# Kernel tuning notes

Measured on AMD Instinct MI355X. Metric: run time of the kernel, lower is better.

The kernel has to match this reference:

```python
import jax, jax.numpy as jnp
import numpy as np
from jax import lax

H = 128

def _lstm_gates(x, h, c, w_ih, w_hh, b_ih, b_hh):
    # PyTorch gate order: i, f, g, o
    g = x @ w_ih.T + h @ w_hh.T + b_ih + b_hh
    i, f, gg, o = jnp.split(g, 4, axis=-1)
    c_new = jax.nn.sigmoid(f) * c + jax.nn.sigmoid(i) * jnp.tanh(gg)
    h_new = jax.nn.sigmoid(o) * jnp.tanh(c_new)
    return h_new, c_new

def _lstm_layer(x_btF, w_ih, w_hh, b_ih, b_hh):
    B = x_btF.shape[0]
    h0 = jnp.zeros((B, H), x_btF.dtype)
    c0 = jnp.zeros((B, H), x_btF.dtype)
    def step(carry, xt):
        h, c = carry
        h, c = _lstm_gates(xt, h, c, w_ih, w_hh, b_ih, b_hh)
        return (h, c), h
    (h_T, c_T), ys = lax.scan(step, (h0, c0), jnp.swapaxes(x_btF, 0, 1))
    return jnp.swapaxes(ys, 0, 1), h_T, c_T

def setup_inputs() -> dict:
    key = jax.random.key(0)
    ks = jax.random.split(key, 20)
    B, T, D, P = 4096, 200, 2, 3
    s = 1.0 / np.sqrt(H)
    u = lambda k, shp: jax.random.uniform(k, shp, jnp.float32, -s, s)
    return {
        'x_hist': jax.random.normal(ks[0], (B, T, D), jnp.float32),
        'params': jax.random.normal(ks[1], (B, P), jnp.float32),
        'pred_len': 200,
        'w_ih0': u(ks[2], (4 * H, D)), 'w_hh0': u(ks[3], (4 * H, H)),
        'b_ih0': u(ks[4], (4 * H,)), 'b_hh0': u(ks[5], (4 * H,)),
        'w_ih1': u(ks[6], (4 * H, H)), 'w_hh1': u(ks[7], (4 * H, H)),
        'b_ih1': u(ks[8], (4 * H,)), 'b_hh1': u(ks[9], (4 * H,)),
        'dec_w_ih': u(ks[10], (4 * H, D + P)), 'dec_w_hh': u(ks[11], (4 * H, H)),
        'dec_b_ih': u(ks[12], (4 * H,)), 'dec_b_hh': u(ks[13], (4 * H,)),
        'proj_w': u(ks[14], (H, P)), 'proj_b': u(ks[15], (H,)),
        'out_w': u(ks[16], (2, H)), 'out_b': u(ks[17], (2,)),
    }

def reference(x_hist, params, pred_len, w_ih0, w_hh0, b_ih0, b_hh0,
              w_ih1, w_hh1, b_ih1, b_hh1, dec_w_ih, dec_w_hh, dec_b_ih,
              dec_b_hh, proj_w, proj_b, out_w, out_b):
    # 2-layer encoder LSTM; only last layer's final (h, c) are used
    y1, _, _ = _lstm_layer(x_hist, w_ih0, w_hh0, b_ih0, b_hh0)
    _, h_n, c_n = _lstm_layer(y1, w_ih1, w_hh1, b_ih1, b_hh1)
    h = h_n + params @ proj_w.T + proj_b
    c = c_n
    cur = x_hist[:, -1, :]
    def step(carry, _):
        h, c, cur = carry
        inp = jnp.concatenate([cur, params], axis=-1)
        h, c = _lstm_gates(inp, h, c, dec_w_ih, dec_w_hh, dec_b_ih, dec_b_hh)
        cur = h @ out_w.T + out_b
        return (h, c, cur), cur
    _, preds = lax.scan(step, (h, c, cur), None, length=pred_len)
    return jnp.swapaxes(preds, 0, 1)  # [B, pred_len, 2]
```

## Files before the change

kernel.cpp:

```cpp
#include <hip/hip_runtime.h>
#include <stdint.h>

typedef __bf16 bf16x8 __attribute__((ext_vector_type(8)));
typedef float  f32x4  __attribute__((ext_vector_type(4)));

#define PRED   200
#define TSTEPS 200
#define NBLK   256

#define ASTR   280
#define ALO    136
#define ABUFE  (16*ASTR*2)
#define W_BYTES 131072
#define A_OFF   W_BYTES
#define LDS_A   (A_OFF + 2*ABUFE)
#define STG_OFF (A_OFF + 2*ABUFE)
#define LDS_C   (STG_OFF + ABUFE)

#define ABUFD  8192
#define LDS_D  (2*ABUFD)

#define STATE_FLOATS ((size_t)NBLK*4*2048)

__device__ __forceinline__ float sigm(float x){ return 1.0f/(1.0f+__expf(-x)); }
__device__ __forceinline__ float tanhx(float x){
  float t=__expf(-2.0f*fabsf(x)); float y=(1.0f-t)/(1.0f+t); return copysignf(y,x);
}
__device__ __forceinline__ bf16x8 hi8(float4 a, float4 b){
  bf16x8 r; r[0]=(__bf16)a.x; r[1]=(__bf16)a.y; r[2]=(__bf16)a.z; r[3]=(__bf16)a.w;
  r[4]=(__bf16)b.x; r[5]=(__bf16)b.y; r[6]=(__bf16)b.z; r[7]=(__bf16)b.w; return r;
}
__device__ __forceinline__ bf16x8 lo8(float4 a, float4 b, bf16x8 h){
  bf16x8 r;
  r[0]=(__bf16)(a.x-(float)h[0]); r[1]=(__bf16)(a.y-(float)h[1]);
  r[2]=(__bf16)(a.z-(float)h[2]); r[3]=(__bf16)(a.w-(float)h[3]);
  r[4]=(__bf16)(b.x-(float)h[4]); r[5]=(__bf16)(b.y-(float)h[5]);
  r[6]=(__bf16)(b.z-(float)h[6]); r[7]=(__bf16)(b.w-(float)h[7]); return r;
}
#define MFMA(A,B,C) __builtin_amdgcn_mfma_f32_16x16x32_bf16((A),(B),(C),0,0,0)

__device__ __forceinline__ int aoff(int row, int col){
  return row*512 + ((((col>>3) ^ (row&7)) << 4) | ((col&7)<<1));
}
__device__ __forceinline__ int frdoff(int c, int qd, int kt, int plane){
  return c*512 + (((((kt<<2)+qd) ^ (c&7)) | (plane<<4)) << 4);
}

__global__ void __launch_bounds__(512,2)
k_l0(const float* __restrict__ xh, const float* __restrict__ wih0,
     const float* __restrict__ whh0, const float* __restrict__ bih0,
     const float* __restrict__ bhh0, float* __restrict__ wsf,
     int chunkStart, int chunkLen, unsigned long long stageFloats)
{
  extern __shared__ char smem[];
  const int tid=threadIdx.x, wv=tid>>6, l=tid&63, c=l&15, qd=l>>4;
  const int hc=wv*16+c, blk=blockIdx.x, r0=blk*16;
  float* stf = wsf + stageFloats;
  #pragma unroll
  for (int i=0;i<16;++i){
    int f=i*8+wv, ntg=f>>2, kt=f&3;
    int g=(ntg&3)*128+(ntg>>2)*16+c, k=kt*32+qd*8;
    const float* s=whh0+g*128+k;
    *(bf16x8*)(smem+f*1024+l*16)=hi8(*(const float4*)s,*(const float4*)(s+4));
  }
  bf16x8 wlo[16];
  #pragma unroll
  for (int tt=0;tt<4;++tt)
    #pragma unroll
    for (int kt=0;kt<4;++kt){
      const float* s=whh0+(size_t)(tt*128+hc)*128+kt*32+qd*8;
      float4 a=*(const float4*)s, b=*(const float4*)(s+4);
      wlo[tt*4+kt]=lo8(a,b,hi8(a,b));
    }
  float b0[4], w0x[4], w0y[4];
  #pragma unroll
  for (int tt=0;tt<4;++tt){
    int g=tt*128+hc;
    b0[tt]=bih0[g]+bhh0[g]; w0x[tt]=wih0[2*g]; w0y[tt]=wih0[2*g+1];
  }
  float c0[4];
  {
    __bf16* B1=(__bf16*)(smem+A_OFF+ABUFE);
    const float* hst=stf+(size_t)(blk*4+0)*2048;
    const float* cst=stf+(size_t)(blk*4+1)*2048;
    #pragma unroll
    for (int i=0;i<4;++i){
      int e=tid*4+i, row=e>>7, col=e&127;
      float v=0.f; if(chunkStart) v=hst[e];
      __bf16 h=(__bf16)v;
      B1[row*ASTR+col]=h; B1[row*ASTR+ALO+col]=(__bf16)(v-(float)h);
    }
    #pragma unroll
    for (int j=0;j<4;++j){ float v=0.f; if(chunkStart) v=cst[(qd*4+j)*128+hc]; c0[j]=v; }
  }
  __syncthreads();
  float hprev[4];
  for (int t=0;t<chunkLen;++t){
    const int p=t&1, tg=chunkStart+t;
    if (t){
      float* h0p=wsf+((size_t)(t-1)*NBLK+blk)*2048;
      #pragma unroll
      for (int j=0;j<4;++j) h0p[(qd*4+j)*128+hc]=hprev[j];
    }
    float2 xv[4];
    #pragma unroll
    for (int j=0;j<4;++j) xv[j]=*(const float2*)(xh+(size_t)(r0+qd*4+j)*400+tg*2);
    f32x4 acc[4];
    #pragma unroll
    for (int tt=0;tt<4;++tt) acc[tt]=(f32x4){b0[tt],b0[tt],b0[tt],b0[tt]};
    const char* Ar=smem+A_OFF+(size_t)(1-p)*ABUFE;
    #pragma unroll
    for (int kt=0;kt<4;++kt){
      bf16x8 ah=*(const bf16x8*)(Ar+(c*ASTR+kt*32+qd*8)*2);
      bf16x8 al=*(const bf16x8*)(Ar+(c*ASTR+ALO+kt*32+qd*8)*2);
      #pragma unroll
      for (int tt=0;tt<4;++tt){
        bf16x8 bh=*(const bf16x8*)(smem+(size_t)((wv*4+tt)*4+kt)*1024+l*16);
        acc[tt]=MFMA(ah,bh,acc[tt]);
        acc[tt]=MFMA(al,bh,acc[tt]);
        acc[tt]=MFMA(ah,wlo[tt*4+kt],acc[tt]);
      }
    }
    __bf16* Aw=(__bf16*)(smem+A_OFF+(size_t)p*ABUFE);
    #pragma unroll
    for (int j=0;j<4;++j){
      float gi=acc[0][j]+xv[j].x*w0x[0]+xv[j].y*w0y[0];
      float gf=acc[1][j]+xv[j].x*w0x[1]+xv[j].y*w0y[1];
      float gg=acc[2][j]+xv[j].x*w0x[2]+xv[j].y*w0y[2];
      float go=acc[3][j]+xv[j].x*w0x[3]+xv[j].y*w0y[3];
      float cn=sigm(gf)*c0[j]+sigm(gi)*tanhx(gg); c0[j]=cn;
      float hn=sigm(go)*tanhx(cn);
      int row=qd*4+j;
      __bf16 hh=(__bf16)hn;
      Aw[row*ASTR+hc]=hh; Aw[row*ASTR+ALO+hc]=(__bf16)(hn-(float)hh);
      hprev[j]=hn;
    }
    __syncthreads();
  }
  {
    float* h0p=wsf+((size_t)(chunkLen-1)*NBLK+blk)*2048;
    #pragma unroll
    for (int j=0;j<4;++j){
      int row=qd*4+j;
      h0p[row*128+hc]=hprev[j];
      stf[(size_t)(blk*4+0)*2048+row*128+hc]=hprev[j];
      stf[(size_t)(blk*4+1)*2048+row*128+hc]=c0[j];
    }
  }
}

__global__ void __launch_bounds__(512,2)
k_l1(const float* __restrict__ wih1, const float* __restrict__ whh1,
     const float* __restrict__ bih1, const float* __restrict__ bhh1,
     float* __restrict__ wsf, int chunkStart, int chunkLen,
     unsigned long long stageFloats)
{
  extern __shared__ char smem[];
  const int tid=threadIdx.x, wv=tid>>6, l=tid&63, c=l&15, qd=l>>4;
  const int hc=wv*16+c, blk=blockIdx.x;
  float* stf = wsf + stageFloats;
  #pragma unroll
  for (int i=0;i<16;++i){
    int f=i*8+wv, ntg=f>>2, kt=f&3;
    int g=(ntg&3)*128+(ntg>>2)*16+c, k=kt*32+qd*8;
    const float* s=wih1+g*128+k;
    *(bf16x8*)(smem+f*1024+l*16)=hi8(*(const float4*)s,*(const float4*)(s+4));
  }
  bf16x8 whh[16], whl[16], wil[16];
  #pragma unroll
  for (int tt=0;tt<4;++tt)
    #pragma unroll
    for (int kt=0;kt<4;++kt){
      const float* s2=whh1+(size_t)(tt*128+hc)*128+kt*32+qd*8;
      float4 a2=*(const float4*)s2, b2=*(const float4*)(s2+4);
      bf16x8 h2=hi8(a2,b2);
      whh[tt*4+kt]=h2; whl[tt*4+kt]=lo8(a2,b2,h2);
      const float* s3=wih1+(size_t)(tt*128+hc)*128+kt*32+qd*8;
      float4 a3=*(const float4*)s3, b3=*(const float4*)(s3+4);
      wil[tt*4+kt]=lo8(a3,b3,hi8(a3,b3));
    }
  float b1v[4];
  #pragma unroll
  for (int tt=0;tt<4;++tt){ int g=tt*128+hc; b1v[tt]=bih1[g]+bhh1[g]; }
  float c1[4];
  {
    __bf16* B1=(__bf16*)(smem+A_OFF+ABUFE);
    const float* hst=stf+(size_t)(blk*4+2)*2048;
    const float* cst=stf+(size_t)(blk*4+3)*2048;
    #pragma unroll
    for (int i=0;i<4;++i){
      int e=tid*4+i, row=e>>7, col=e&127;
      float v=0.f; if(chunkStart) v=hst[e];
      __bf16 h=(__bf16)v;
      B1[row*ASTR+col]=h; B1[row*ASTR+ALO+col]=(__bf16)(v-(float)h);
    }
    #pragma unroll
    for (int j=0;j<4;++j){ float v=0.f; if(chunkStart) v=cst[(qd*4+j)*128+hc]; c1[j]=v; }
  }
  float4 r4=*(const float4*)(wsf+((size_t)0*NBLK+blk)*2048+tid*4);
  __syncthreads();
  for (int t=0;t<chunkLen;++t){
    const int p=t&1;
    {
      __bf16* ST=(__bf16*)(smem+STG_OFF);
      int e=tid*4, row=e>>7, col=e&127;
      #pragma unroll
      for (int i=0;i<4;++i){
        float v=((const float*)&r4)[i]; __bf16 h=(__bf16)v;
        ST[row*ASTR+col+i]=h; ST[row*ASTR+ALO+col+i]=(__bf16)(v-(float)h);
      }
    }
    if (t+1<chunkLen) r4=*(const float4*)(wsf+((size_t)(t+1)*NBLK+blk)*2048+tid*4);
    __syncthreads();
    f32x4 acc[4];
    #pragma unroll
    for (int tt=0;tt<4;++tt) acc[tt]=(f32x4){b1v[tt],b1v[tt],b1v[tt],b1v[tt]};
    const char* Ar=smem+A_OFF+(size_t)(1-p)*ABUFE;
    const char* Sr=smem+STG_OFF;
    #pragma unroll
    for (int kt=0;kt<4;++kt){
      bf16x8 a0h=*(const bf16x8*)(Sr+(c*ASTR+kt*32+qd*8)*2);
      bf16x8 a0l=*(const bf16x8*)(Sr+(c*ASTR+ALO+kt*32+qd*8)*2);
      bf16x8 a1h=*(const bf16x8*)(Ar+(c*ASTR+kt*32+qd*8)*2);
      bf16x8 a1l=*(const bf16x8*)(Ar+(c*ASTR+ALO+kt*32+qd*8)*2);
      #pragma unroll
      for (int tt=0;tt<4;++tt){
        bf16x8 bh=*(const bf16x8*)(smem+(size_t)((wv*4+tt)*4+kt)*1024+l*16);
        acc[tt]=MFMA(a0h,bh,acc[tt]);
        acc[tt]=MFMA(a0l,bh,acc[tt]);
        acc[tt]=MFMA(a0h,wil[tt*4+kt],acc[tt]);
        acc[tt]=MFMA(a1h,whh[tt*4+kt],acc[tt]);
        acc[tt]=MFMA(a1l,whh[tt*4+kt],acc[tt]);
        acc[tt]=MFMA(a1h,whl[tt*4+kt],acc[tt]);
      }
    }
    __bf16* Aw=(__bf16*)(smem+A_OFF+(size_t)p*ABUFE);
    #pragma unroll
    for (int j=0;j<4;++j){
      float cn=sigm(acc[1][j])*c1[j]+sigm(acc[0][j])*tanhx(acc[2][j]); c1[j]=cn;
      float hn=sigm(acc[3][j])*tanhx(cn);
      int row=qd*4+j;
      __bf16 hh=(__bf16)hn;
      Aw[row*ASTR+hc]=hh; Aw[row*ASTR+ALO+hc]=(__bf16)(hn-(float)hh);
      if (t==chunkLen-1){
        stf[(size_t)(blk*4+2)*2048+row*128+hc]=hn;
        stf[(size_t)(blk*4+3)*2048+row*128+hc]=cn;
      }
    }
    __syncthreads();
  }
}

__global__ void __launch_bounds__(512,1)
k_dec(const float* __restrict__ xh, const float* __restrict__ pprm,
      const float* __restrict__ dwihp, const float* __restrict__ dwhh,
      const float* __restrict__ dbih, const float* __restrict__ dbhh,
      const float* __restrict__ pw, const float* __restrict__ pb,
      const float* __restrict__ ow, const float* __restrict__ ob,
      const float* __restrict__ wsf, float* __restrict__ out,
      unsigned long long stageFloats)
{
  extern __shared__ char smem[];
  const int tid=threadIdx.x, wv=tid>>6, l=tid&63, c=l&15, qd=l>>4;
  const int hc=wv*16+c, blk=blockIdx.x, r0=blk*16;
  const float* stf = wsf + stageFloats;
  float ob0=ob[0], ob1=ob[1];
  float prm[4][3];
  #pragma unroll
  for (int j=0;j<4;++j){
    size_t r=(size_t)(r0+qd*4+j);
    prm[j][0]=pprm[r*3+0]; prm[j][1]=pprm[r*3+1]; prm[j][2]=pprm[r*3+2];
  }
  float ptF[4][4], dw0[4], dw1[4];
  #pragma unroll
  for (int tt=0;tt<4;++tt){
    int g=tt*128+hc;
    float db=dbih[g]+dbhh[g];
    dw0[tt]=dwihp[g*5+0]; dw1[tt]=dwihp[g*5+1];
    #pragma unroll
    for (int j=0;j<4;++j)
      ptF[tt][j]=db+prm[j][0]*dwihp[g*5+2]+prm[j][1]*dwihp[g*5+3]+prm[j][2]*dwihp[g*5+4]
                 +dw0[tt]*ob0+dw1[tt]*ob1;
  }
  bf16x8 whi[16], wlo[16];
  #pragma unroll
  for (int tt=0;tt<4;++tt)
    #pragma unroll
    for (int kt=0;kt<4;++kt){
      int g=tt*128+hc, k=kt*32+qd*8;
      float4 a=*(const float4*)(dwhh+(size_t)g*128+k), b=*(const float4*)(dwhh+(size_t)g*128+k+4);
      float4 o0a=*(const float4*)(ow+k),     o0b=*(const float4*)(ow+k+4);
      float4 o1a=*(const float4*)(ow+128+k), o1b=*(const float4*)(ow+128+k+4);
      a.x+=dw0[tt]*o0a.x+dw1[tt]*o1a.x; a.y+=dw0[tt]*o0a.y+dw1[tt]*o1a.y;
      a.z+=dw0[tt]*o0a.z+dw1[tt]*o1a.z; a.w+=dw0[tt]*o0a.w+dw1[tt]*o1a.w;
      b.x+=dw0[tt]*o0b.x+dw1[tt]*o1b.x; b.y+=dw0[tt]*o0b.y+dw1[tt]*o1b.y;
      b.z+=dw0[tt]*o0b.z+dw1[tt]*o1b.z; b.w+=dw0[tt]*o0b.w+dw1[tt]*o1b.w;
      whi[tt*4+kt]=hi8(a,b); wlo[tt*4+kt]=lo8(a,b,whi[tt*4+kt]);
    }
  bf16x8 owh[4], owl[4];
  #pragma unroll
  for (int kt=0;kt<4;++kt){
    int cc=(c<2)?c:0;
    const float* s=ow+cc*128+kt*32+qd*8;
    float4 a=*(const float4*)s, b=*(const float4*)(s+4);
    if (c>=2){ a=(float4){0,0,0,0}; b=(float4){0,0,0,0}; }
    owh[kt]=hi8(a,b); owl[kt]=lo8(a,b,owh[kt]);
  }
  const float* h1s=stf+(size_t)(blk*4+2)*2048;
  const float* c1s=stf+(size_t)(blk*4+3)*2048;
  float c1[4], cx0[4], cx1[4];
  {
    float prj0=pw[hc*3+0], prj1=pw[hc*3+1], prj2=pw[hc*3+2], prjb=pb[hc];
    char* B0=smem;
    #pragma unroll
    for (int j=0;j<4;++j){
      int row=qd*4+j;
      float hd=h1s[row*128+hc]+prm[j][0]*prj0+prm[j][1]*prj1+prm[j][2]*prj2+prjb;
      __bf16 h=(__bf16)hd;
      *(__bf16*)(B0+aoff(row,hc))=h;
      *(__bf16*)(B0+aoff(row,hc+128))=(__bf16)(hd-(float)h);
      c1[j]=c1s[row*128+hc];
      float2 xx=*(const float2*)(xh+(size_t)(r0+row)*400+398);
      cx0[j]=xx.x; cx1[j]=xx.y;
    }
  }
  __syncthreads();
  float corr0[4], corr1[4];
  {
    const char* Ar=smem;
    f32x4 pv={0.f,0.f,0.f,0.f};
    #pragma unroll
    for (int kt=0;kt<4;++kt){
      bf16x8 ah=*(const bf16x8*)(Ar+frdoff(c,qd,kt,0));
      bf16x8 al=*(const bf16x8*)(Ar+frdoff(c,qd,kt,1));
      pv=MFMA(ah,owh[kt],pv); pv=MFMA(al,owh[kt],pv); pv=MFMA(ah,owl[kt],pv);
    }
    #pragma unroll
    for (int j=0;j<4;++j){
      float p0=__shfl(pv[j], (l&48),   64);
      float p1=__shfl(pv[j], (l&48)|1, 64);
      corr0[j]=cx0[j]-(p0+ob0);
      corr1[j]=cx1[j]-(p1+ob1);
    }
  }
  f32x4 pvPrev={0.f,0.f,0.f,0.f};
  for (int s=0;s<PRED;++s){
    const int q=s&1;
    if (s>=2 && wv==0 && c<2){
      float obv=c?ob1:ob0;
      #pragma unroll
      for (int j=0;j<4;++j)
        out[(size_t)(r0+qd*4+j)*400+(s-2)*2+c]=pvPrev[j]+obv;
    }
    const char* Ar=smem+(size_t)q*ABUFD;
    bf16x8 ah[4], al[4];
    #pragma unroll
    for (int kt=0;kt<4;++kt){
      ah[kt]=*(const bf16x8*)(Ar+frdoff(c,qd,kt,0));
      al[kt]=*(const bf16x8*)(Ar+frdoff(c,qd,kt,1));
    }
    f32x4 aA[4], aB[4];
    #pragma unroll
    for (int tt=0;tt<4;++tt){ aA[tt]=(f32x4){ptF[tt][0],ptF[tt][1],ptF[tt][2],ptF[tt][3]}; aB[tt]=(f32x4){0.f,0.f,0.f,0.f}; }
    #pragma unroll
    for (int kt=0;kt<4;++kt)
      #pragma unroll
      for (int tt=0;tt<4;++tt){
        f32x4* tgt=(kt<2)?&aA[tt]:&aB[tt];
        *tgt=MFMA(ah[kt],whi[tt*4+kt],*tgt);
        *tgt=MFMA(al[kt],whi[tt*4+kt],*tgt);
        *tgt=MFMA(ah[kt],wlo[tt*4+kt],*tgt);
      }
    f32x4 pv={0.f,0.f,0.f,0.f};
    if (wv==0){
      #pragma unroll
      for (int kt=0;kt<4;++kt){
        pv=MFMA(ah[kt],owh[kt],pv); pv=MFMA(al[kt],owh[kt],pv); pv=MFMA(ah[kt],owl[kt],pv);
      }
    }
    char* Aw=smem+(size_t)(1-q)*ABUFD;
    #pragma unroll
    for (int j=0;j<4;++j){
      float gi=aA[0][j]+aB[0][j];
      float gf=aA[1][j]+aB[1][j];
      float gg=aA[2][j]+aB[2][j];
      float go=aA[3][j]+aB[3][j];
      if (s==0){
        gi+=corr0[j]*dw0[0]+corr1[j]*dw1[0];
        gf+=corr0[j]*dw0[1]+corr1[j]*dw1[1];
        gg+=corr0[j]*dw0[2]+corr1[j]*dw1[2];
        go+=corr0[j]*dw0[3]+corr1[j]*dw1[3];
      }
      float cn=sigm(gf)*c1[j]+sigm(gi)*tanhx(gg); c1[j]=cn;
      float hn=sigm(go)*tanhx(cn);
      int row=qd*4+j;
      __bf16 hh=(__bf16)hn;
      *(__bf16*)(Aw+aoff(row,hc))=hh;
      *(__bf16*)(Aw+aoff(row,hc+128))=(__bf16)(hn-(float)hh);
    }
    if (wv==0) pvPrev=pv;
    __syncthreads();
  }
  if (wv==0 && c<2){
    float obv=c?ob1:ob0;
    #pragma unroll
    for (int j=0;j<4;++j)
      out[(size_t)(r0+qd*4+j)*400+(PRED-2)*2+c]=pvPrev[j]+obv;
  }
  if (wv==0){
    const char* Ar=smem+(size_t)(PRED&1)*ABUFD;
    f32x4 pv={0.f,0.f,0.f,0.f};
    #pragma unroll
    for (int kt=0;kt<4;++kt){
      bf16x8 ah=*(const bf16x8*)(Ar+frdoff(c,qd,kt,0));
      bf16x8 al=*(const bf16x8*)(Ar+frdoff(c,qd,kt,1));
      pv=MFMA(ah,owh[kt],pv); pv=MFMA(al,owh[kt],pv); pv=MFMA(ah,owl[kt],pv);
    }
    if (c<2){
      float obv=c?ob1:ob0;
      #pragma unroll
      for (int j=0;j<4;++j)
        out[(size_t)(r0+qd*4+j)*400+(PRED-1)*2+c]=pv[j]+obv;
    }
  }
}

extern "C" void kernel_launch(void* const* d_in, const int* in_sizes, int n_in,
                              void* d_out, int out_size, void* d_ws, size_t ws_size,
                              hipStream_t stream)
{
  (void)out_size;
  const int base = (n_in >= 19 && in_sizes[2] == 1) ? 3 : 2;
  const float* xh   = (const float*)d_in[0];
  const float* prm  = (const float*)d_in[1];
  const float* wih0 = (const float*)d_in[base+0];
  const float* whh0 = (const float*)d_in[base+1];
  const float* bih0 = (const float*)d_in[base+2];
  const float* bhh0 = (const float*)d_in[base+3];
  const float* wih1 = (const float*)d_in[base+4];
  const float* whh1 = (const float*)d_in[base+5];
  const float* bih1 = (const float*)d_in[base+6];
  const float* bhh1 = (const float*)d_in[base+7];
  const float* dwih = (const float*)d_in[base+8];
  const float* dwhh = (const float*)d_in[base+9];
  const float* dbih = (const float*)d_in[base+10];
  const float* dbhh = (const float*)d_in[base+11];
  const float* pw   = (const float*)d_in[base+12];
  const float* pb   = (const float*)d_in[base+13];
  const float* ow   = (const float*)d_in[base+14];
  const float* ob   = (const float*)d_in[base+15];
  float* wsf = (float*)d_ws;

  size_t wsFloats = ws_size / 4;
  size_t avail = (wsFloats > STATE_FLOATS) ? (wsFloats - STATE_FLOATS) : 0;
  int chunkLen = (int)(avail / ((size_t)NBLK * 2048));
  if (chunkLen > 50) chunkLen = 50;
  if (chunkLen < 1)  chunkLen = 1;
  unsigned long long stageFloats = (unsigned long long)chunkLen * NBLK * 2048;

  hipFuncSetAttribute((const void*)k_l0, hipFuncAttributeMaxDynamicSharedMemorySize, LDS_A);
  hipFuncSetAttribute((const void*)k_l1, hipFuncAttributeMaxDynamicSharedMemorySize, LDS_C);

  for (int k0 = 0; k0 < TSTEPS; k0 += chunkLen){
    int len = chunkLen; if (k0 + len > TSTEPS) len = TSTEPS - k0;
    k_l0<<<NBLK,512,LDS_A,stream>>>(xh, wih0, whh0, bih0, bhh0, wsf, k0, len, stageFloats);
    k_l1<<<NBLK,512,LDS_C,stream>>>(wih1, whh1, bih1, bhh1, wsf, k0, len, stageFloats);
  }
  k_dec<<<NBLK,512,LDS_D,stream>>>(xh, prm, dwih, dwhh, dbih, dbhh,
                                   pw, pb, ow, ob, wsf, (float*)d_out, stageFloats);
}
```

Before: 1.878 ms.

## Keep layer-0 weights in registers and stream layer-1 input directly into fragments

Layer 0 now holds both the hi and lo bf16 splits of W_hh in registers instead of reading the hi part from LDS, so its LDS footprint shrinks to just the h double buffer. The x input is prefetched one step ahead. Layer 1 drops the LDS staging buffer and its extra barrier: each lane loads its own A-fragment of the layer-0 output from global memory and splits it into hi/lo in registers, prefetching the next step. Layer 1's launch bounds drop to one block per CU to make room for the larger register footprint, which risks lower occupancy and spills.

After: 2.828 ms. +50.6%, slower.

```diff
diff --git a/kernel.cpp b/kernel.cpp
--- a/kernel.cpp
+++ b/kernel.cpp
@@ -11,11 +11,10 @@
 #define ASTR   280
 #define ALO    136
 #define ABUFE  (16*ASTR*2)
+#define LDS_A  (2*ABUFE)
 #define W_BYTES 131072
 #define A_OFF   W_BYTES
-#define LDS_A   (A_OFF + 2*ABUFE)
-#define STG_OFF (A_OFF + 2*ABUFE)
-#define LDS_C   (STG_OFF + ABUFE)
+#define LDS_C   (A_OFF + 2*ABUFE)
 
 #define ABUFD  8192
 #define LDS_D  (2*ABUFD)
@@ -56,21 +55,15 @@
   const int tid=threadIdx.x, wv=tid>>6, l=tid&63, c=l&15, qd=l>>4;
   const int hc=wv*16+c, blk=blockIdx.x, r0=blk*16;
   float* stf = wsf + stageFloats;
-  #pragma unroll
-  for (int i=0;i<16;++i){
-    int f=i*8+wv, ntg=f>>2, kt=f&3;
-    int g=(ntg&3)*128+(ntg>>2)*16+c, k=kt*32+qd*8;
-    const float* s=whh0+g*128+k;
-    *(bf16x8*)(smem+f*1024+l*16)=hi8(*(const float4*)s,*(const float4*)(s+4));
-  }
-  bf16x8 wlo[16];
+  bf16x8 whi[16], wlo[16];
   #pragma unroll
   for (int tt=0;tt<4;++tt)
     #pragma unroll
     for (int kt=0;kt<4;++kt){
       const float* s=whh0+(size_t)(tt*128+hc)*128+kt*32+qd*8;
       float4 a=*(const float4*)s, b=*(const float4*)(s+4);
-      wlo[tt*4+kt]=lo8(a,b,hi8(a,b));
+      bf16x8 h=hi8(a,b);
+      whi[tt*4+kt]=h; wlo[tt*4+kt]=lo8(a,b,h);
     }
   float b0[4], w0x[4], w0y[4];
   #pragma unroll
@@ -80,7 +73,7 @@
   }
   float c0[4];
   {
-    __bf16* B1=(__bf16*)(smem+A_OFF+ABUFE);
+    __bf16* B1=(__bf16*)(smem+ABUFE);
     const float* hst=stf+(size_t)(blk*4+0)*2048;
     const float* cst=stf+(size_t)(blk*4+1)*2048;
     #pragma unroll
@@ -95,6 +88,9 @@
   }
   __syncthreads();
   float hprev[4];
+  float2 xv[4];
+  #pragma unroll
+  for (int j=0;j<4;++j) xv[j]=*(const float2*)(xh+(size_t)(r0+qd*4+j)*400+chunkStart*2);
   for (int t=0;t<chunkLen;++t){
     const int p=t&1, tg=chunkStart+t;
     if (t){
@@ -102,26 +98,29 @@
       #pragma unroll
       for (int j=0;j<4;++j) h0p[(qd*4+j)*128+hc]=hprev[j];
     }
-    float2 xv[4];
-    #pragma unroll
-    for (int j=0;j<4;++j) xv[j]=*(const float2*)(xh+(size_t)(r0+qd*4+j)*400+tg*2);
+    float2 xn[4];
+    #pragma unroll
+    for (int j=0;j<4;++j) xn[j]=(float2){0.f,0.f};
+    if (t+1<chunkLen){
+      #pragma unroll
+      for (int j=0;j<4;++j) xn[j]=*(const float2*)(xh+(size_t)(r0+qd*4+j)*400+(tg+1)*2);
+    }
     f32x4 acc[4];
     #pragma unroll
     for (int tt=0;tt<4;++tt) acc[tt]=(f32x4){b0[tt],b0[tt],b0[tt],b0[tt]};
-    const char* Ar=smem+A_OFF+(size_t)(1-p)*ABUFE;
+    const char* Ar=smem+(size_t)(1-p)*ABUFE;
     #pragma unroll
     for (int kt=0;kt<4;++kt){
       bf16x8 ah=*(const bf16x8*)(Ar+(c*ASTR+kt*32+qd*8)*2);
       bf16x8 al=*(const bf16x8*)(Ar+(c*ASTR+ALO+kt*32+qd*8)*2);
       #pragma unroll
       for (int tt=0;tt<4;++tt){
-        bf16x8 bh=*(const bf16x8*)(smem+(size_t)((wv*4+tt)*4+kt)*1024+l*16);
-        acc[tt]=MFMA(ah,bh,acc[tt]);
-        acc[tt]=MFMA(al,bh,acc[tt]);
+        acc[tt]=MFMA(ah,whi[tt*4+kt],acc[tt]);
+        acc[tt]=MFMA(al,whi[tt*4+kt],acc[tt]);
         acc[tt]=MFMA(ah,wlo[tt*4+kt],acc[tt]);
       }
     }
-    __bf16* Aw=(__bf16*)(smem+A_OFF+(size_t)p*ABUFE);
+    __bf16* Aw=(__bf16*)(smem+(size_t)p*ABUFE);
     #pragma unroll
     for (int j=0;j<4;++j){
       float gi=acc[0][j]+xv[j].x*w0x[0]+xv[j].y*w0y[0];
@@ -135,6 +134,8 @@
       Aw[row*ASTR+hc]=hh; Aw[row*ASTR+ALO+hc]=(__bf16)(hn-(float)hh);
       hprev[j]=hn;
     }
+    #pragma unroll
+    for (int j=0;j<4;++j) xv[j]=xn[j];
     __syncthreads();
   }
   {
@@ -149,7 +150,7 @@
   }
 }
 
-__global__ void __launch_bounds__(512,2)
+__global__ void __launch_bounds__(512,1)
 k_l1(const float* __restrict__ wih1, const float* __restrict__ whh1,
      const float* __restrict__ bih1, const float* __restrict__ bhh1,
      float* __restrict__ wsf, int chunkStart, int chunkLen,
@@ -197,38 +198,46 @@
     #pragma unroll
     for (int j=0;j<4;++j){ float v=0.f; if(chunkStart) v=cst[(qd*4+j)*128+hc]; c1[j]=v; }
   }
-  float4 r4=*(const float4*)(wsf+((size_t)0*NBLK+blk)*2048+tid*4);
+  float4 xq[8];
+  {
+    const float* h0b=wsf+((size_t)0*NBLK+blk)*2048+c*128;
+    #pragma unroll
+    for (int kt=0;kt<4;++kt){
+      xq[2*kt  ]=*(const float4*)(h0b+kt*32+qd*8);
+      xq[2*kt+1]=*(const float4*)(h0b+kt*32+qd*8+4);
+    }
+  }
   __syncthreads();
   for (int t=0;t<chunkLen;++t){
     const int p=t&1;
-    {
-      __bf16* ST=(__bf16*)(smem+STG_OFF);
-      int e=tid*4, row=e>>7, col=e&127;
-      #pragma unroll
-      for (int i=0;i<4;++i){
-        float v=((const float*)&r4)[i]; __bf16 h=(__bf16)v;
-        ST[row*ASTR+col+i]=h; ST[row*ASTR+ALO+col+i]=(__bf16)(v-(float)h);
-      }
-    }
-    if (t+1<chunkLen) r4=*(const float4*)(wsf+((size_t)(t+1)*NBLK+blk)*2048+tid*4);
-    __syncthreads();
+    bf16x8 a0h[4], a0l[4];
+    #pragma unroll
+    for (int kt=0;kt<4;++kt){
+      a0h[kt]=hi8(xq[2*kt],xq[2*kt+1]);
+      a0l[kt]=lo8(xq[2*kt],xq[2*kt+1],a0h[kt]);
+    }
+    if (t+1<chunkLen){
+      const float* h0b=wsf+((size_t)(t+1)*NBLK+blk)*2048+c*128;
+      #pragma unroll
+      for (int kt=0;kt<4;++kt){
+        xq[2*kt  ]=*(const float4*)(h0b+kt*32+qd*8);
+        xq[2*kt+1]=*(const float4*)(h0b+kt*32+qd*8+4);
+      }
+    }
     f32x4 acc[4];
     #pragma unroll
     for (int tt=0;tt<4;++tt) acc[tt]=(f32x4){b1v[tt],b1v[tt],b1v[tt],b1v[tt]};
     const char* Ar=smem+A_OFF+(size_t)(1-p)*ABUFE;
-    const char* Sr=smem+STG_OFF;
-    #pragma unroll
-    for (int kt=0;kt<4;++kt){
-      bf16x8 a0h=*(const bf16x8*)(Sr+(c*ASTR+kt*32+qd*8)*2);
-      bf16x8 a0l=*(const bf16x8*)(Sr+(c*ASTR+ALO+kt*32+qd*8)*2);
+    #pragma unroll
+    for (int kt=0;kt<4;++kt){
       bf16x8 a1h=*(const bf16x8*)(Ar+(c*ASTR+kt*32+qd*8)*2);
       bf16x8 a1l=*(const bf16x8*)(Ar+(c*ASTR+ALO+kt*32+qd*8)*2);
       #pragma unroll
       for (int tt=0;tt<4;++tt){
         bf16x8 bh=*(const bf16x8*)(smem+(size_t)((wv*4+tt)*4+kt)*1024+l*16);
-        acc[tt]=MFMA(a0h,bh,acc[tt]);
-        acc[tt]=MFMA(a0l,bh,acc[tt]);
-        acc[tt]=MFMA(a0h,wil[tt*4+kt],acc[tt]);
+        acc[tt]=MFMA(a0h[kt],bh,acc[tt]);
+        acc[tt]=MFMA(a0l[kt],bh,acc[tt]);
+        acc[tt]=MFMA(a0h[kt],wil[tt*4+kt],acc[tt]);
         acc[tt]=MFMA(a1h,whh[tt*4+kt],acc[tt]);
         acc[tt]=MFMA(a1l,whh[tt*4+kt],acc[tt]);
         acc[tt]=MFMA(a1h,whl[tt*4+kt],acc[tt]);
```
